# Optimization experiments

Hardware: AMD Instinct MI355X
Metric: run time of the kernel (lower is better)

The kernel has to match this reference:

```python
import math
import jax, jax.numpy as jnp
import numpy as np

D_MODEL = 1024
N_STATE = 64
DT_MIN, DT_MAX = 1e-3, 1e-1
L_LEN = 2048


def setup_inputs() -> dict:
    key = jax.random.key(0)
    k_c, k_d, k_dt = jax.random.split(key, 3)
    n = jnp.arange(N_STATE, dtype=jnp.float32)
    A_real = -0.5 * jnp.ones((N_STATE,), dtype=jnp.float32)
    A_imag = math.pi * (n + 0.5)
    B = jnp.broadcast_to(jnp.sqrt(2.0 * n + 1.0)[:, None], (N_STATE, D_MODEL)).astype(jnp.float32)
    # C stored as real view (d_model, N, 2) like torch.view_as_real
    C = (jax.random.normal(k_c, (D_MODEL, N_STATE, 2), dtype=jnp.float32) * 0.5)
    D = jax.random.normal(k_d, (D_MODEL,), dtype=jnp.float32)
    log_dt = (jax.random.uniform(k_dt, (D_MODEL,), dtype=jnp.float32)
              * (math.log(DT_MAX) - math.log(DT_MIN)) + math.log(DT_MIN))
    return {"A_real": A_real, "A_imag": A_imag, "B": B, "C": C, "D": D,
            "log_dt": log_dt, "L": L_LEN}


def reference(A_real, A_imag, B, C, D, log_dt, L):
    dt = jnp.exp(log_dt)                              # (d,)
    A = A_real + 1j * A_imag                          # (N,) complex
    dtA = dt[:, None] * A[None, :]                    # (d, N)
    A_bar = (1.0 + dtA / 2.0) / (1.0 - dtA / 2.0)     # bilinear discretization
    B_bar = dt[:, None] * B.T / (1.0 - dtA / 2.0)     # (d, N)
    Cc = C[..., 0] + 1j * C[..., 1]                   # (d, N)
    ks = jnp.arange(L, dtype=jnp.float32)             # (L,)
    # Vandermonde powers: (d, N, L) complex — the big intermediate
    A_pow = A_bar[:, :, None] ** ks[None, None, :]
    K = jnp.real(jnp.sum((Cc * B_bar)[:, :, None] * A_pow, axis=1))  # (d, L)
    K = K.at[:, 0].add(D)                             # D * delta[0] skip term
    return K
```

## Files before the change

kernel.cpp:

```cpp
#include <hip/hip_runtime.h>
#include <math.h>

#define D_MODEL 1024
#define N_STATE 64
#define L_LEN   2048

__global__ __launch_bounds__(256) void s4d_setup(
    const float* __restrict__ A_real, const float* __restrict__ A_imag,
    const float* __restrict__ B, const float* __restrict__ C,
    const float* __restrict__ log_dt, float* __restrict__ par)
{
    const int id = blockIdx.x * 256 + threadIdx.x;
    const int d = id >> 6;
    const int n = id & 63;

    const double dt = exp((double)log_dt[d]);
    const double zr = 0.5 * dt * (double)A_real[n];
    const double zi = 0.5 * dt * (double)A_imag[n];
    const double dr = 1.0 - zr, di = -zi;
    const double inv = 1.0 / (dr*dr + di*di);
    const double nr = 1.0 + zr, ni = zi;
    const double sr = (nr*dr + ni*di) * inv;
    const double si = (ni*dr - nr*di) * inv;
    const double dtB = dt * (double)B[n*D_MODEL + d];
    const double br = dtB * dr * inv;
    const double bi = dtB * zi * inv;
    const double cr = (double)C[(d*N_STATE + n)*2 + 0];
    const double ci = (double)C[(d*N_STATE + n)*2 + 1];
    const double wr = cr*br - ci*bi;
    const double wi = cr*bi + ci*br;

    const double INV2PI = 0.15915494309189535;
    const double threv = atan2(si, sr) * INV2PI;
    const double la    = 0.5 * log2(sr*sr + si*si);
    const double w2    = wr*wr + wi*wi;
    const double lw    = 0.5 * log2(fmax(w2, 1e-60));
    const double phrev = atan2(wi, wr) * INV2PI;

    const double th_hi = nearbyint(threv * 4096.0) * (1.0 / 4096.0);
    const double la_hi = nearbyint(la    * 4096.0) * (1.0 / 4096.0);

    double pr = sr, pq = si;
    #pragma unroll
    for (int k = 0; k < 4; ++k) {
        double a2 = pr*pr - pq*pq;
        double b2 = 2.0*pr*pq;
        pr = a2; pq = b2;
    }

    float4 p0, p1;
    p0.x = (float)th_hi;
    p0.y = (float)(threv - th_hi);
    p0.z = (float)phrev;
    p0.w = (float)la_hi;
    p1.x = (float)(la - la_hi);
    p1.y = (float)lw;
    p1.z = (float)(2.0 * pr);
    p1.w = (float)(pr*pr + pq*pq);
    float4* o = (float4*)(par + (size_t)id * 8);
    o[0] = p0;
    o[1] = p1;
}

__device__ __forceinline__ float eval_term(float lf,
                                           float th_hi, float th_lo, float ph0,
                                           float la_hi, float la_lo, float lw) {
    float amp = exp2f(fmaf(lf, la_hi, fmaf(lf, la_lo, lw)));
    float f1  = __builtin_amdgcn_fractf(lf * th_hi);
    float ph  = __builtin_amdgcn_fractf(f1 + fmaf(lf, th_lo, ph0));
    return amp * __builtin_amdgcn_cosf(ph);
}

__global__ __launch_bounds__(256) void s4d_main(
    const float* __restrict__ par, const float* __restrict__ Dv,
    float* __restrict__ out)
{
    const int d = blockIdx.x;
    const int t = threadIdx.x;
    const int wv   = t >> 6;
    const int lane = t & 63;
    const int q    = lane >> 4;
    const int g    = lane & 15;
    const int lbase = wv * 512 + g;

    const float4* pp = (const float4*)(par + (size_t)d * (N_STATE * 8));
    const float lf0 = (float)lbase;
    const float lf1 = (float)(lbase + 16);

    float y0[16], y1[16], ar[16], am[16];
    #pragma unroll
    for (int c = 0; c < 16; ++c) {
        const int n = (c << 2) | q;
        const float4 a = pp[2*n];
        const float4 b = pp[2*n + 1];
        ar[c] = b.z;
        am[c] = b.w;
        y0[c] = eval_term(lf0, a.x, a.y, a.z, a.w, b.x, b.y);
        y1[c] = eval_term(lf1, a.x, a.y, a.z, a.w, b.x, b.y);
    }

    const float dval = Dv[d];
    float* __restrict__ op = out + (size_t)d * L_LEN;

    #pragma unroll
    for (int i = 0; i < 32; ++i) {
        float r8[8];
        #pragma unroll
        for (int k = 0; k < 8; ++k) r8[k] = y0[2*k] + y0[2*k+1];
        float r4a = r8[0] + r8[1], r4b = r8[2] + r8[3];
        float r4c = r8[4] + r8[5], r4d = r8[6] + r8[7];
        float sum = (r4a + r4b) + (r4c + r4d);
        sum += __shfl_xor(sum, 16);
        sum += __shfl_xor(sum, 32);
        if (q == (i & 3)) {
            const int l = lbase + 16 * i;
            float v = sum;
            if (l == 0) v += dval;
            op[l] = v;
        }
        #pragma unroll
        for (int c = 0; c < 16; ++c) {
            float yn = fmaf(ar[c], y1[c], -(am[c] * y0[c]));
            y0[c] = y1[c];
            y1[c] = yn;
        }
    }
}

extern "C" void kernel_launch(void* const* d_in, const int* in_sizes, int n_in,
                              void* d_out, int out_size, void* d_ws, size_t ws_size,
                              hipStream_t stream) {
    const float* A_real = (const float*)d_in[0];
    const float* A_imag = (const float*)d_in[1];
    const float* B      = (const float*)d_in[2];
    const float* C      = (const float*)d_in[3];
    const float* Dv     = (const float*)d_in[4];
    const float* log_dt = (const float*)d_in[5];
    float* out = (float*)d_out;
    float* par = (float*)d_ws;
    (void)in_sizes; (void)n_in; (void)ws_size; (void)out_size;

    s4d_setup<<<dim3(D_MODEL * N_STATE / 256), dim3(256), 0, stream>>>(
        A_real, A_imag, B, C, log_dt, par);
    s4d_main<<<dim3(D_MODEL), dim3(256), 0, stream>>>(par, Dv, out);
}
```

Before: 85.81 us.

## Factor Vandermonde sum into split-bf16 MFMA matmul over block decomposition of L

```diff
diff --git a/kernel.cpp b/kernel.cpp
--- a/kernel.cpp
+++ b/kernel.cpp
@@ -4,6 +4,10 @@
 #define D_MODEL 1024
 #define N_STATE 64
 #define L_LEN   2048
+#define PAR_STRIDE 8
+
+typedef __attribute__((ext_vector_type(8))) short  short8;
+typedef __attribute__((ext_vector_type(4))) float  f32x4;
 
 __global__ __launch_bounds__(256) void s4d_setup(
     const float* __restrict__ A_real, const float* __restrict__ A_imag,
@@ -40,14 +44,6 @@
     const double th_hi = nearbyint(threv * 4096.0) * (1.0 / 4096.0);
     const double la_hi = nearbyint(la    * 4096.0) * (1.0 / 4096.0);
 
-    double pr = sr, pq = si;
-    #pragma unroll
-    for (int k = 0; k < 4; ++k) {
-        double a2 = pr*pr - pq*pq;
-        double b2 = 2.0*pr*pq;
-        pr = a2; pq = b2;
-    }
-
     float4 p0, p1;
     p0.x = (float)th_hi;
     p0.y = (float)(threv - th_hi);
@@ -55,75 +51,155 @@
     p0.w = (float)la_hi;
     p1.x = (float)(la - la_hi);
     p1.y = (float)lw;
-    p1.z = (float)(2.0 * pr);
-    p1.w = (float)(pr*pr + pq*pq);
-    float4* o = (float4*)(par + (size_t)id * 8);
+    p1.z = 0.0f;
+    p1.w = 0.0f;
+    float4* o = (float4*)(par + (size_t)id * PAR_STRIDE);
     o[0] = p0;
     o[1] = p1;
 }
 
-__device__ __forceinline__ float eval_term(float lf,
-                                           float th_hi, float th_lo, float ph0,
-                                           float la_hi, float la_lo, float lw) {
-    float amp = exp2f(fmaf(lf, la_hi, fmaf(lf, la_lo, lw)));
-    float f1  = __builtin_amdgcn_fractf(lf * th_hi);
-    float ph  = __builtin_amdgcn_fractf(f1 + fmaf(lf, th_lo, ph0));
-    return amp * __builtin_amdgcn_cosf(ph);
+__device__ __forceinline__ unsigned short bf16_rne(float x) {
+    unsigned int u = __float_as_uint(x);
+    return (unsigned short)((u + 0x7FFFu + ((u >> 16) & 1u)) >> 16);
+}
+__device__ __forceinline__ float bf16_f(unsigned short h) {
+    return __uint_as_float((unsigned int)h << 16);
 }
 
 __global__ __launch_bounds__(256) void s4d_main(
     const float* __restrict__ par, const float* __restrict__ Dv,
     float* __restrict__ out)
 {
+    __shared__ __align__(16) float s_par[N_STATE][8];
+    __shared__ __align__(16) short s_u[4 * 64 * 72];
+    __shared__ __align__(16) short s_v[4 * 32 * 72];
+
     const int d = blockIdx.x;
     const int t = threadIdx.x;
-    const int wv   = t >> 6;
+
+    if (t < 64) {
+        const float4* g = (const float4*)(par + ((size_t)d * 64 + t) * PAR_STRIDE);
+        *(float4*)&s_par[t][0] = g[0];
+        *(float4*)&s_par[t][4] = g[1];
+    }
+    __syncthreads();
+
+    {
+        const int b = t & 63, g = t >> 6;
+        const float lf = (float)b;
+        #pragma unroll
+        for (int half = 0; half < 2; ++half) {
+            short8 prh, prl, pih, pil;
+            #pragma unroll
+            for (int nn = 0; nn < 8; ++nn) {
+                const int n = (g << 4) + (half << 3) + nn;
+                const float th_hi = s_par[n][0], th_lo = s_par[n][1];
+                const float ph0   = s_par[n][2], la_hi = s_par[n][3];
+                const float la_lo = s_par[n][4], lw    = s_par[n][5];
+                float amp = exp2f(fmaf(lf, la_hi, fmaf(lf, la_lo, lw)));
+                float f1  = __builtin_amdgcn_fractf(lf * th_hi);
+                float ph  = __builtin_amdgcn_fractf(f1 + fmaf(lf, th_lo, ph0));
+                float zr  = amp * __builtin_amdgcn_cosf(ph);
+                float zi  = amp * __builtin_amdgcn_sinf(ph);
+                unsigned short rh = bf16_rne(zr);
+                unsigned short rl = bf16_rne(zr - bf16_f(rh));
+                float niz = -zi;
+                unsigned short ih = bf16_rne(niz);
+                unsigned short il = bf16_rne(niz - bf16_f(ih));
+                prh[nn] = (short)rh; prl[nn] = (short)rl;
+                pih[nn] = (short)ih; pil[nn] = (short)il;
+            }
+            const int base = b * 72 + (g << 4) + (half << 3);
+            *(short8*)&s_u[0 * 4608 + base] = prh;
+            *(short8*)&s_u[1 * 4608 + base] = prl;
+            *(short8*)&s_u[2 * 4608 + base] = pih;
+            *(short8*)&s_u[3 * 4608 + base] = pil;
+        }
+    }
+    {
+        const int a = t & 31, h = t >> 5;
+        const float lf = (float)(a << 6);
+        short8 prh, prl, pih, pil;
+        #pragma unroll
+        for (int nn = 0; nn < 8; ++nn) {
+            const int n = (h << 3) + nn;
+            const float th_hi = s_par[n][0], th_lo = s_par[n][1];
+            const float la_hi = s_par[n][3], la_lo = s_par[n][4];
+            float amp = exp2f(fmaf(lf, la_hi, lf * la_lo));
+            float f1  = __builtin_amdgcn_fractf(lf * th_hi);
+            float ph  = __builtin_amdgcn_fractf(f1 + lf * th_lo);
+            float vr  = amp * __builtin_amdgcn_cosf(ph);
+            float vi  = amp * __builtin_amdgcn_sinf(ph);
+            unsigned short rh = bf16_rne(vr);
+            unsigned short rl = bf16_rne(vr - bf16_f(rh));
+            unsigned short ih = bf16_rne(vi);
+            unsigned short il = bf16_rne(vi - bf16_f(ih));
+            prh[nn] = (short)rh; prl[nn] = (short)rl;
+            pih[nn] = (short)ih; pil[nn] = (short)il;
+        }
+        const int base = a * 72 + (h << 3);
+        *(short8*)&s_v[0 * 2304 + base] = prh;
+        *(short8*)&s_v[1 * 2304 + base] = prl;
+        *(short8*)&s_v[2 * 2304 + base] = pih;
+        *(short8*)&s_v[3 * 2304 + base] = pil;
+    }
+    __syncthreads();
+
+    const int w    = t >> 6;
     const int lane = t & 63;
-    const int q    = lane >> 4;
-    const int g    = lane & 15;
-    const int lbase = wv * 512 + g;
-
-    const float4* pp = (const float4*)(par + (size_t)d * (N_STATE * 8));
-    const float lf0 = (float)lbase;
-    const float lf1 = (float)(lbase + 16);
-
-    float y0[16], y1[16], ar[16], am[16];
+    const int col  = lane & 15;
+    const int grp  = lane >> 4;
+    const int brow = (w << 4) + col;
+
+    f32x4 acc0 = {0.f, 0.f, 0.f, 0.f};
+    f32x4 acc1 = {0.f, 0.f, 0.f, 0.f};
+
     #pragma unroll
-    for (int c = 0; c < 16; ++c) {
-        const int n = (c << 2) | q;
-        const float4 a = pp[2*n];
-        const float4 b = pp[2*n + 1];
-        ar[c] = b.z;
-        am[c] = b.w;
-        y0[c] = eval_term(lf0, a.x, a.y, a.z, a.w, b.x, b.y);
-        y1[c] = eval_term(lf1, a.x, a.y, a.z, a.w, b.x, b.y);
-    }
-
-    const float dval = Dv[d];
+    for (int ksp = 0; ksp < 2; ++ksp) {
+        const int k0 = (ksp << 5) + (grp << 3);
+        const int ub = brow * 72 + k0;
+        const short8 urh = *(const short8*)&s_u[0 * 4608 + ub];
+        const short8 url = *(const short8*)&s_u[1 * 4608 + ub];
+        const short8 uih = *(const short8*)&s_u[2 * 4608 + ub];
+        const short8 uil = *(const short8*)&s_u[3 * 4608 + ub];
+        {
+            const int vb = col * 72 + k0;
+            const short8 vrh = *(const short8*)&s_v[0 * 2304 + vb];
+            const short8 vrl = *(const short8*)&s_v[1 * 2304 + vb];
+            const short8 vih = *(const short8*)&s_v[2 * 2304 + vb];
+            const short8 vil = *(const short8*)&s_v[3 * 2304 + vb];
+            acc0 = __builtin_amdgcn_mfma_f32_16x16x32_bf16(vrh, urh, acc0, 0, 0, 0);
+            acc0 = __builtin_amdgcn_mfma_f32_16x16x32_bf16(vrh, url, acc0, 0, 0, 0);
+            acc0 = __builtin_amdgcn_mfma_f32_16x16x32_bf16(vrl, urh, acc0, 0, 0, 0);
+            acc0 = __builtin_amdgcn_mfma_f32_16x16x32_bf16(vih, uih, acc0, 0, 0, 0);
+            acc0 = __builtin_amdgcn_mfma_f32_16x16x32_bf16(vih, uil, acc0, 0, 0, 0);
+            acc0 = __builtin_amdgcn_mfma_f32_16x16x32_bf16(vil, uih, acc0, 0, 0, 0);
+        }
+        {
+            const int vb = (16 + col) * 72 + k0;
+            const short8 vrh = *(const short8*)&s_v[0 * 2304 + vb];
+            const short8 vrl = *(const short8*)&s_v[1 * 2304 + vb];
+            const short8 vih = *(const short8*)&s_v[2 * 2304 + vb];
+            const short8 vil = *(const short8*)&s_v[3 * 2304 + vb];
+            acc1 = __builtin_amdgcn_mfma_f32_16x16x32_bf16(vrh, urh, acc1, 0, 0, 0);
+            acc1 = __builtin_amdgcn_mfma_f32_16x16x32_bf16(vrh, url, acc1, 0, 0, 0);
+            acc1 = __builtin_amdgcn_mfma_f32_16x16x32_bf16(vrl, urh, acc1, 0, 0, 0);
+            acc1 = __builtin_amdgcn_mfma_f32_16x16x32_bf16(vih, uih, acc1, 0, 0, 0);
+            acc1 = __builtin_amdgcn_mfma_f32_16x16x32_bf16(vih, uil, acc1, 0, 0, 0);
+            acc1 = __builtin_amdgcn_mfma_f32_16x16x32_bf16(vil, uih, acc1, 0, 0, 0);
+        }
+    }
+
     float* __restrict__ op = out + (size_t)d * L_LEN;
-
+    const int b = brow;
     #pragma unroll
-    for (int i = 0; i < 32; ++i) {
-        float r8[8];
-        #pragma unroll
-        for (int k = 0; k < 8; ++k) r8[k] = y0[2*k] + y0[2*k+1];
-        float r4a = r8[0] + r8[1], r4b = r8[2] + r8[3];
-        float r4c = r8[4] + r8[5], r4d = r8[6] + r8[7];
-        float sum = (r4a + r4b) + (r4c + r4d);
-        sum += __shfl_xor(sum, 16);
-        sum += __shfl_xor(sum, 32);
-        if (q == (i & 3)) {
-            const int l = lbase + 16 * i;
-            float v = sum;
-            if (l == 0) v += dval;
-            op[l] = v;
-        }
-        #pragma unroll
-        for (int c = 0; c < 16; ++c) {
-            float yn = fmaf(ar[c], y1[c], -(am[c] * y0[c]));
-            y0[c] = y1[c];
-            y1[c] = yn;
-        }
+    for (int r = 0; r < 4; ++r) {
+        const int a0 = (grp << 2) + r;
+        float v0 = acc0[r];
+        if (r == 0 && t == 0) v0 += Dv[d];
+        op[(a0 << 6) + b] = v0;
+        const int a1 = a0 + 16;
+        op[(a1 << 6) + b] = acc1[r];
     }
 }
 
```

Result: faster. 79.43 us (-7.4%).
